# Optimization experiments

Hardware: AMD Instinct MI355X
Metric: run time of the kernel (lower is better)

## Reference

```python
import jax, jax.numpy as jnp
import numpy as np

N_BITS = 14
L = 1 << N_BITS
B, C_IN, C_OUT = 32, 32, 64

def _neigh_idx():
    # (L, n_bits): index j flipped at bit b -> j ^ (1<<b)
    s = jnp.arange(L)
    return jnp.stack([s ^ (1 << b) for b in range(N_BITS)], axis=1)

def setup_inputs() -> dict:
    key = jax.random.key(0)
    k1, k2, k3, k4 = jax.random.split(key, 4)
    x = jax.random.normal(k1, (B, C_IN, L), dtype=jnp.float32)
    w_self = jnp.ones((), dtype=jnp.float32)
    w_bits = jax.random.normal(k2, (N_BITS,), dtype=jnp.float32) * 0.1
    # Conv1d(kernel_size=1) weight squeezed to (C_out, C_in)
    mix_w = jax.random.normal(k3, (C_OUT, C_IN), dtype=jnp.float32) * (1.0 / np.sqrt(C_IN))
    mix_b = jax.random.normal(k4, (C_OUT,), dtype=jnp.float32) * 0.01
    return {"x": x, "w_self": w_self, "w_bits": w_bits, "mix_w": mix_w, "mix_b": mix_b}

def reference(x, w_self, w_bits, mix_w, mix_b):
    n_bits = w_bits.shape[0]
    idx = _neigh_idx()                          # (L, n_bits), int32
    xn = x[:, :, idx]                           # (B, C, L, n_bits) XOR-neighbor gather
    neigh_sum = jnp.einsum('bclk,k->bcl', xn, w_bits)
    y = w_self * x + neigh_sum
    y = y / (1.0 + n_bits)                      # agg == 'mean'
    # 1x1 conv mix: (B,C,L) x (C_out,C_in) -> (B,C_out,L)
    return jnp.einsum('bcl,oc->bol', y, mix_w) + mix_b[None, :, None]
```

## Files before the change

### kernel.cpp

```cpp
#include <hip/hip_runtime.h>

#define TILE  256
#define CIN   32
#define COUT  64
#define LSIZE 16384
#define NBITS 14
#define MWPAD 68

typedef float vfloat4 __attribute__((ext_vector_type(4)));

__global__ __launch_bounds__(256, 3)
void hamming_fused(const float* __restrict__ x,
                   const float* __restrict__ w_self,
                   const float* __restrict__ w_bits,
                   const float* __restrict__ mix_w,
                   const float* __restrict__ mix_b,
                   float* __restrict__ out)
{
    __shared__ float xs[CIN][TILE];
    __shared__ float mws[CIN][MWPAD];

    const int tid = threadIdx.x;

    const int d    = blockIdx.x;
    const int xcd  = d & 7;
    const int j    = d >> 3;
    const int b    = xcd * 4 + (j >> 6);
    const int tile = j & 63;
    const int base = tile * TILE;
    const float* xb = x + (size_t)b * CIN * LSIZE;

    #pragma unroll
    for (int i = 0; i < 8; ++i) {
        int g = tid + i * 256;
        mws[g & 31][g >> 5] = mix_w[g];
    }

    #pragma unroll
    for (int i = 0; i < 8; ++i) {
        int idx = tid + i * 256;
        int r  = idx >> 6;
        int c4 = (idx & 63) << 2;
        *(float4*)&xs[r][c4] =
            *(const float4*)(xb + (size_t)r * LSIZE + base + c4);
    }
    __syncthreads();

    const float ws = w_self[0];
    float wb[NBITS];
    #pragma unroll
    for (int k = 0; k < NBITS; ++k) wb[k] = w_bits[k];

    const int tx   = tid & 63;
    const int grp  = tid >> 6;
    const int colb = tx << 2;
    const int c0   = grp * 8;
    const int gb   = base + colb;

    float4 yreg[8];
    #pragma unroll
    for (int cc = 0; cc < 8; ++cc) {
        const int c = c0 + cc;
        const float* xr = xb + (size_t)c * LSIZE;

        float4 g0 = *(const float4*)(xr + (gb ^ 256));
        float4 g1 = *(const float4*)(xr + (gb ^ 512));
        float4 g2 = *(const float4*)(xr + (gb ^ 1024));
        float4 g3 = *(const float4*)(xr + (gb ^ 2048));
        float4 g4 = *(const float4*)(xr + (gb ^ 4096));
        float4 g5 = *(const float4*)(xr + (gb ^ 8192));

        float4 s = *(float4*)&xs[c][colb];
        float4 a;
        a.x = ws * s.x + wb[0] * s.y + wb[1] * s.z;
        a.y = ws * s.y + wb[0] * s.x + wb[1] * s.w;
        a.z = ws * s.z + wb[0] * s.w + wb[1] * s.x;
        a.w = ws * s.w + wb[0] * s.z + wb[1] * s.y;

        #pragma unroll
        for (int k = 2; k < 8; ++k) {
            float4 tp = *(float4*)&xs[c][colb ^ (1 << k)];
            a.x += wb[k] * tp.x;
            a.y += wb[k] * tp.y;
            a.z += wb[k] * tp.z;
            a.w += wb[k] * tp.w;
        }

        a.x += wb[8]*g0.x + wb[9]*g1.x + wb[10]*g2.x + wb[11]*g3.x + wb[12]*g4.x + wb[13]*g5.x;
        a.y += wb[8]*g0.y + wb[9]*g1.y + wb[10]*g2.y + wb[11]*g3.y + wb[12]*g4.y + wb[13]*g5.y;
        a.z += wb[8]*g0.z + wb[9]*g1.z + wb[10]*g2.z + wb[11]*g3.z + wb[12]*g4.z + wb[13]*g5.z;
        a.w += wb[8]*g0.w + wb[9]*g1.w + wb[10]*g2.w + wb[11]*g3.w + wb[12]*g4.w + wb[13]*g5.w;

        yreg[cc].x = a.x * (1.0f / 15.0f);
        yreg[cc].y = a.y * (1.0f / 15.0f);
        yreg[cc].z = a.z * (1.0f / 15.0f);
        yreg[cc].w = a.w * (1.0f / 15.0f);
    }

    #pragma unroll
    for (int cc = 0; cc < 8; ++cc)
        *(float4*)&xs[c0 + cc][colb] = yreg[cc];
    __syncthreads();

    const int o0 = grp * 16;

    float4 acc[16];
    #pragma unroll
    for (int jj = 0; jj < 16; ++jj) {
        float bias = mix_b[o0 + jj];
        acc[jj] = make_float4(bias, bias, bias, bias);
    }

    #pragma unroll 4
    for (int c = 0; c < CIN; ++c) {
        float4 yv = *(float4*)&xs[c][colb];
        #pragma unroll
        for (int j4 = 0; j4 < 4; ++j4) {
            float4 m = *(float4*)&mws[c][o0 + j4 * 4];
            acc[j4*4+0].x += m.x * yv.x; acc[j4*4+0].y += m.x * yv.y;
            acc[j4*4+0].z += m.x * yv.z; acc[j4*4+0].w += m.x * yv.w;
            acc[j4*4+1].x += m.y * yv.x; acc[j4*4+1].y += m.y * yv.y;
            acc[j4*4+1].z += m.y * yv.z; acc[j4*4+1].w += m.y * yv.w;
            acc[j4*4+2].x += m.z * yv.x; acc[j4*4+2].y += m.z * yv.y;
            acc[j4*4+2].z += m.z * yv.z; acc[j4*4+2].w += m.z * yv.w;
            acc[j4*4+3].x += m.w * yv.x; acc[j4*4+3].y += m.w * yv.y;
            acc[j4*4+3].z += m.w * yv.z; acc[j4*4+3].w += m.w * yv.w;
        }
    }

    float* ob = out + (size_t)b * COUT * LSIZE;
    #pragma unroll
    for (int jj = 0; jj < 16; ++jj) {
        vfloat4 v; v.x = acc[jj].x; v.y = acc[jj].y; v.z = acc[jj].z; v.w = acc[jj].w;
        vfloat4* p = (vfloat4*)(ob + (size_t)(o0 + jj) * LSIZE + base + colb);
        __builtin_nontemporal_store(v, p);
    }
}

extern "C" void kernel_launch(void* const* d_in, const int* in_sizes, int n_in,
                              void* d_out, int out_size, void* d_ws, size_t ws_size,
                              hipStream_t stream) {
    const float* x      = (const float*)d_in[0];
    const float* w_self = (const float*)d_in[1];
    const float* w_bits = (const float*)d_in[2];
    const float* mix_w  = (const float*)d_in[3];
    const float* mix_b  = (const float*)d_in[4];
    float* out = (float*)d_out;

    hamming_fused<<<dim3(2048), 256, 0, stream>>>(x, w_self, w_bits, mix_w, mix_b, out);
}
```

Baseline: 217.3 us.

## Halve spatial tile to 128 and double blocks for higher occupancy

```diff
diff --git a/kernel.cpp b/kernel.cpp
--- a/kernel.cpp
+++ b/kernel.cpp
@@ -1,6 +1,6 @@
 #include <hip/hip_runtime.h>
 
-#define TILE  256
+#define TILE  128
 #define CIN   32
 #define COUT  64
 #define LSIZE 16384
@@ -9,7 +9,7 @@
 
 typedef float vfloat4 __attribute__((ext_vector_type(4)));
 
-__global__ __launch_bounds__(256, 3)
+__global__ __launch_bounds__(256, 6)
 void hamming_fused(const float* __restrict__ x,
                    const float* __restrict__ w_self,
                    const float* __restrict__ w_bits,
@@ -25,8 +25,8 @@
     const int d    = blockIdx.x;
     const int xcd  = d & 7;
     const int j    = d >> 3;
-    const int b    = xcd * 4 + (j >> 6);
-    const int tile = j & 63;
+    const int b    = xcd * 4 + (j >> 7);
+    const int tile = j & 127;
     const int base = tile * TILE;
     const float* xb = x + (size_t)b * CIN * LSIZE;
 
@@ -37,38 +37,41 @@
     }
 
     #pragma unroll
-    for (int i = 0; i < 8; ++i) {
+    for (int i = 0; i < 4; ++i) {
         int idx = tid + i * 256;
-        int r  = idx >> 6;
-        int c4 = (idx & 63) << 2;
+        int r  = idx >> 5;
+        int c4 = (idx & 31) << 2;
         *(float4*)&xs[r][c4] =
             *(const float4*)(xb + (size_t)r * LSIZE + base + c4);
     }
     __syncthreads();
 
-    const float ws = w_self[0];
+    const float ws = w_self[0] * (1.0f / 15.0f);
     float wb[NBITS];
     #pragma unroll
-    for (int k = 0; k < NBITS; ++k) wb[k] = w_bits[k];
+    for (int k = 0; k < NBITS; ++k) wb[k] = w_bits[k] * (1.0f / 15.0f);
 
-    const int tx   = tid & 63;
-    const int grp  = tid >> 6;
-    const int colb = tx << 2;
-    const int c0   = grp * 8;
+    const int lane = tid & 63;
+    const int wv   = tid >> 6;
+    const int quad = lane & 31;
+    const int half = lane >> 5;
+    const int colb = quad << 2;
     const int gb   = base + colb;
+    const int c0   = wv * 8 + half * 4;
 
-    float4 yreg[8];
+    float4 yreg[4];
     #pragma unroll
-    for (int cc = 0; cc < 8; ++cc) {
+    for (int cc = 0; cc < 4; ++cc) {
         const int c = c0 + cc;
         const float* xr = xb + (size_t)c * LSIZE;
 
-        float4 g0 = *(const float4*)(xr + (gb ^ 256));
-        float4 g1 = *(const float4*)(xr + (gb ^ 512));
-        float4 g2 = *(const float4*)(xr + (gb ^ 1024));
-        float4 g3 = *(const float4*)(xr + (gb ^ 2048));
-        float4 g4 = *(const float4*)(xr + (gb ^ 4096));
-        float4 g5 = *(const float4*)(xr + (gb ^ 8192));
+        float4 g0 = *(const float4*)(xr + (gb ^ 128));
+        float4 g1 = *(const float4*)(xr + (gb ^ 256));
+        float4 g2 = *(const float4*)(xr + (gb ^ 512));
+        float4 g3 = *(const float4*)(xr + (gb ^ 1024));
+        float4 g4 = *(const float4*)(xr + (gb ^ 2048));
+        float4 g5 = *(const float4*)(xr + (gb ^ 4096));
+        float4 g6 = *(const float4*)(xr + (gb ^ 8192));
 
         float4 s = *(float4*)&xs[c][colb];
         float4 a;
@@ -78,7 +81,7 @@
         a.w = ws * s.w + wb[0] * s.z + wb[1] * s.y;
 
         #pragma unroll
-        for (int k = 2; k < 8; ++k) {
+        for (int k = 2; k < 7; ++k) {
             float4 tp = *(float4*)&xs[c][colb ^ (1 << k)];
             a.x += wb[k] * tp.x;
             a.y += wb[k] * tp.y;
@@ -86,36 +89,36 @@
             a.w += wb[k] * tp.w;
         }
 
-        a.x += wb[8]*g0.x + wb[9]*g1.x + wb[10]*g2.x + wb[11]*g3.x + wb[12]*g4.x + wb[13]*g5.x;
-        a.y += wb[8]*g0.y + wb[9]*g1.y + wb[10]*g2.y + wb[11]*g3.y + wb[12]*g4.y + wb[13]*g5.y;
-        a.z += wb[8]*g0.z + wb[9]*g1.z + wb[10]*g2.z + wb[11]*g3.z + wb[12]*g4.z + wb[13]*g5.z;
-        a.w += wb[8]*g0.w + wb[9]*g1.w + wb[10]*g2.w + wb[11]*g3.w + wb[12]*g4.w + wb[13]*g5.w;
+        a.x += wb[7]*g0.x + wb[8]*g1.x + wb[9]*g2.x + wb[10]*g3.x + wb[11]*g4.x + wb[12]*g5.x + wb[13]*g6.x;
+        a.y += wb[7]*g0.y + wb[8]*g1.y + wb[9]*g2.y + wb[10]*g3.y + wb[11]*g4.y + wb[12]*g5.y + wb[13]*g6.y;
+        a.z += wb[7]*g0.z + wb[8]*g1.z + wb[9]*g2.z + wb[10]*g3.z + wb[11]*g4.z + wb[12]*g5.z + wb[13]*g6.z;
+        a.w += wb[7]*g0.w + wb[8]*g1.w + wb[9]*g2.w + wb[10]*g3.w + wb[11]*g4.w + wb[12]*g5.w + wb[13]*g6.w;
 
-        yreg[cc].x = a.x * (1.0f / 15.0f);
-        yreg[cc].y = a.y * (1.0f / 15.0f);
-        yreg[cc].z = a.z * (1.0f / 15.0f);
-        yreg[cc].w = a.w * (1.0f / 15.0f);
+        yreg[cc] = a;
     }
 
     #pragma unroll
-    for (int cc = 0; cc < 8; ++cc)
+    for (int cc = 0; cc < 4; ++cc)
         *(float4*)&xs[c0 + cc][colb] = yreg[cc];
     __syncthreads();
 
-    const int o0 = grp * 16;
+    const int qa   = tid & 31;
+    const int og   = tid >> 5;
+    const int o0   = og * 8;
+    const int cl2  = qa << 2;
 
-    float4 acc[16];
+    float4 acc[8];
     #pragma unroll
-    for (int jj = 0; jj < 16; ++jj) {
+    for (int jj = 0; jj < 8; ++jj) {
         float bias = mix_b[o0 + jj];
         acc[jj] = make_float4(bias, bias, bias, bias);
     }
 
     #pragma unroll 4
     for (int c = 0; c < CIN; ++c) {
-        float4 yv = *(float4*)&xs[c][colb];
+        float4 yv = *(float4*)&xs[c][cl2];
         #pragma unroll
-        for (int j4 = 0; j4 < 4; ++j4) {
+        for (int j4 = 0; j4 < 2; ++j4) {
             float4 m = *(float4*)&mws[c][o0 + j4 * 4];
             acc[j4*4+0].x += m.x * yv.x; acc[j4*4+0].y += m.x * yv.y;
             acc[j4*4+0].z += m.x * yv.z; acc[j4*4+0].w += m.x * yv.w;
@@ -130,9 +133,9 @@
 
     float* ob = out + (size_t)b * COUT * LSIZE;
     #pragma unroll
-    for (int jj = 0; jj < 16; ++jj) {
+    for (int jj = 0; jj < 8; ++jj) {
         vfloat4 v; v.x = acc[jj].x; v.y = acc[jj].y; v.z = acc[jj].z; v.w = acc[jj].w;
-        vfloat4* p = (vfloat4*)(ob + (size_t)(o0 + jj) * LSIZE + base + colb);
+        vfloat4* p = (vfloat4*)(ob + (size_t)(o0 + jj) * LSIZE + base + cl2);
         __builtin_nontemporal_store(v, p);
     }
 }
@@ -147,5 +150,5 @@
     const float* mix_b  = (const float*)d_in[4];
     float* out = (float*)d_out;
 
-    hamming_fused<<<dim3(2048), 256, 0, stream>>>(x, w_self, w_bits, mix_w, mix_b, out);
+    hamming_fused<<<dim3(4096), 256, 0, stream>>>(x, w_self, w_bits, mix_w, mix_b, out);
 }
```

Measured after the change: 218.8 us. Within noise of the previous version (+0.7%).
